# Kernel optimization log

Hardware: AMD Instinct MI355X
Metric: run time of the kernel (lower is better)

The kernel has to match this reference:

```python
import jax, jax.numpy as jnp
import numpy as np

D, H, FF, EPS = 1024, 16, 4096, 1e-5

def _ln(x, g, b):
    m = jnp.mean(x, axis=-1, keepdims=True)
    v = jnp.var(x, axis=-1, keepdims=True)
    return (x - m) * jax.lax.rsqrt(v + EPS) * g + b

def setup_inputs() -> dict:
    key = jax.random.key(0)
    ks = jax.random.split(key, 8)
    b, t = 2, 2048
    return {
        "x": jax.random.normal(ks[0], (b, t, D), jnp.float32),
        "prev_attn": jax.random.normal(ks[1], (b, H, t, t), jnp.float32) * 0.1,
        "w_qkv": jax.random.normal(ks[2], (D, 3 * D), jnp.float32) * (D ** -0.5),
        "w_out": jax.random.normal(ks[3], (D, D), jnp.float32) * (D ** -0.5),
        "w1": jax.random.normal(ks[4], (D, FF), jnp.float32) * (D ** -0.5),
        "b1": jnp.zeros((FF,), jnp.float32),
        "w2": jax.random.normal(ks[5], (FF, D), jnp.float32) * (FF ** -0.5),
        "b2": jnp.zeros((D,), jnp.float32),
        "g1": jnp.ones((D,), jnp.float32),
        "be1": jnp.zeros((D,), jnp.float32),
        "g2": jnp.ones((D,), jnp.float32),
        "be2": jnp.zeros((D,), jnp.float32),
    }

def reference(x, prev_attn, w_qkv, w_out, w1, b1, w2, b2, g1, be1, g2, be2):
    b, t, d = x.shape
    h, hd = H, d // H
    scale = hd ** -0.5
    qkv = _ln(x, g1, be1) @ w_qkv                       # [b,t,3d]
    q, k, v = jnp.split(qkv, 3, axis=-1)
    q, k, v = [z.reshape(b, t, h, hd).transpose(0, 2, 1, 3) for z in (q, k, v)]
    attn = jnp.einsum('bhid,bhjd->bhij', q, k) * scale + prev_attn
    attn = jax.nn.softmax(attn, axis=-1)                # [b,h,t,t]
    out = jnp.einsum('bhij,bhjd->bhid', attn, v).transpose(0, 2, 1, 3).reshape(b, t, d)
    x = x + out @ w_out
    hdn = _ln(x, g2, be2)
    ffn = jax.nn.gelu(hdn @ w1 + b1, approximate=False) @ w2 + b2
    x = x + ffn
    return (x, jax.lax.stop_gradient(attn))
```

## Files before the change

### kernel.cpp

```cpp
#include <hip/hip_runtime.h>
#include <hip/hip_bf16.h>
#include <math.h>

#define T_SEQ 2048
#define D_MODEL 1024
#define N_HEADS 16
#define HD 64
#define FF_DIM 4096
#define N_ROWS 4096
#define LDQKV 3072

typedef __bf16 bf16x8 __attribute__((ext_vector_type(8)));
typedef float f32x4 __attribute__((ext_vector_type(4)));

__device__ __forceinline__ unsigned short f2bf(float f) {
  union { float f; unsigned u; } v; v.f = f;
  unsigned r = v.u + 0x7FFFu + ((v.u >> 16) & 1u);
  return (unsigned short)(r >> 16);
}
__device__ __forceinline__ float bf2f(unsigned short u) {
  union { unsigned u; float f; } v; v.u = ((unsigned)u) << 16;
  return v.f;
}

__device__ __forceinline__ void gld_lds16(const void* g, void* l) {
  __builtin_amdgcn_global_load_lds(
      (const __attribute__((address_space(1))) unsigned int*)g,
      (__attribute__((address_space(3))) unsigned int*)l, 16, 0, 0);
}

__global__ __launch_bounds__(256) void transpose_w(const float* __restrict__ src,
                                                   unsigned short* __restrict__ dst,
                                                   int R, int C) {
  __shared__ float tile[32][33];
  int c0 = blockIdx.x * 32, r0 = blockIdx.y * 32;
  int tx = threadIdx.x & 31, ty = threadIdx.x >> 5;
#pragma unroll
  for (int i = 0; i < 32; i += 8)
    tile[ty + i][tx] = src[(size_t)(r0 + ty + i) * C + c0 + tx];
  __syncthreads();
#pragma unroll
  for (int i = 0; i < 32; i += 8)
    dst[(size_t)(c0 + ty + i) * R + r0 + tx] = f2bf(tile[tx][ty + i]);
}

__global__ __launch_bounds__(256) void ln_kernel(const float* __restrict__ x,
                                                 const float* __restrict__ g,
                                                 const float* __restrict__ be,
                                                 unsigned short* __restrict__ out) {
  int row = blockIdx.x;
  float4 v = ((const float4*)(x + (size_t)row * D_MODEL))[threadIdx.x];
  float s = v.x + v.y + v.z + v.w;
  float ss = v.x * v.x + v.y * v.y + v.z * v.z + v.w * v.w;
#pragma unroll
  for (int o = 32; o; o >>= 1) { s += __shfl_down(s, o); ss += __shfl_down(ss, o); }
  __shared__ float red[8];
  int wid = threadIdx.x >> 6, lane = threadIdx.x & 63;
  if (lane == 0) { red[wid] = s; red[4 + wid] = ss; }
  __syncthreads();
  if (threadIdx.x == 0) {
    float S0 = red[0] + red[1] + red[2] + red[3];
    float S1 = red[4] + red[5] + red[6] + red[7];
    float m = S0 * (1.0f / D_MODEL);
    red[0] = m;
    red[1] = rsqrtf(S1 * (1.0f / D_MODEL) - m * m + 1e-5f);
  }
  __syncthreads();
  float m = red[0], inv = red[1];
  float4 gv = ((const float4*)g)[threadIdx.x];
  float4 bv = ((const float4*)be)[threadIdx.x];
  ushort4 o;
  o.x = f2bf((v.x - m) * inv * gv.x + bv.x);
  o.y = f2bf((v.y - m) * inv * gv.y + bv.y);
  o.z = f2bf((v.z - m) * inv * gv.z + bv.z);
  o.w = f2bf((v.w - m) * inv * gv.w + bv.w);
  ((ushort4*)(out + (size_t)row * D_MODEL))[threadIdx.x] = o;
}

template <int EPI>
__global__ __launch_bounds__(256) void gemm_bt(const unsigned short* __restrict__ A,
                                               const unsigned short* __restrict__ Bt,
                                               int M, int N, int K,
                                               void* __restrict__ outp,
                                               const float* __restrict__ bias,
                                               const float* __restrict__ res) {
  __shared__ __align__(16) unsigned short As[128 * 32];
  __shared__ __align__(16) unsigned short Bs[128 * 32];
  int tid = threadIdx.x;
  int m0 = blockIdx.x * 128, n0 = blockIdx.y * 128;
  int w = tid >> 6, l = tid & 63;
  int wm = w >> 1, wn = w & 1;
  int lr = l & 15, lg = l >> 4;
  f32x4 acc[4][4] = {};
  const unsigned short* ap0 = A + (size_t)(m0 + (tid >> 2)) * K + (tid & 3) * 8;
  const unsigned short* ap1 = ap0 + (size_t)64 * K;
  const unsigned short* bp0 = Bt + (size_t)(n0 + (tid >> 2)) * K + (tid & 3) * 8;
  const unsigned short* bp1 = bp0 + (size_t)64 * K;
  unsigned short* la0 = As + (tid & ~63) * 8;
  unsigned short* la1 = As + (256 + (tid & ~63)) * 8;
  unsigned short* lb0 = Bs + (tid & ~63) * 8;
  unsigned short* lb1 = Bs + (256 + (tid & ~63)) * 8;
  for (int k0 = 0; k0 < K; k0 += 32) {
    gld_lds16(ap0, la0);
    gld_lds16(ap1, la1);
    gld_lds16(bp0, lb0);
    gld_lds16(bp1, lb1);
    ap0 += 32; ap1 += 32; bp0 += 32; bp1 += 32;
    __syncthreads();
    bf16x8 af[4], bfr[4];
#pragma unroll
    for (int i = 0; i < 4; i++) {
      af[i] = *(const bf16x8*)(As + (wm * 64 + i * 16 + lr) * 32 + lg * 8);
      bfr[i] = *(const bf16x8*)(Bs + (wn * 64 + i * 16 + lr) * 32 + lg * 8);
    }
#pragma unroll
    for (int i = 0; i < 4; i++)
#pragma unroll
      for (int j = 0; j < 4; j++)
        acc[i][j] = __builtin_amdgcn_mfma_f32_16x16x32_bf16(af[i], bfr[j], acc[i][j], 0, 0, 0);
    __syncthreads();
  }
#pragma unroll
  for (int i = 0; i < 4; i++) {
#pragma unroll
    for (int j = 0; j < 4; j++) {
      int col = n0 + wn * 64 + j * 16 + lr;
#pragma unroll
      for (int r = 0; r < 4; r++) {
        int row = m0 + wm * 64 + i * 16 + lg * 4 + r;
        size_t idx = (size_t)row * N + col;
        float v = acc[i][j][r];
        if (EPI == 0) {
          ((unsigned short*)outp)[idx] = f2bf(v);
        } else if (EPI == 1) {
          ((float*)outp)[idx] = res[idx] + v;
        } else if (EPI == 2) {
          float t = v + bias[col];
          ((unsigned short*)outp)[idx] = f2bf(0.5f * t * (1.0f + erff(t * 0.70710678f)));
        } else {
          ((float*)outp)[idx] = v + bias[col] + res[idx];
        }
      }
    }
  }
}

__global__ __launch_bounds__(256) void repack_kv(const unsigned short* __restrict__ qkv,
                                                 unsigned short* __restrict__ kt,
                                                 unsigned short* __restrict__ vt2) {
  __shared__ unsigned short tile[64][66];
  int bh = blockIdx.x >> 5, tt = blockIdx.x & 31;
  int b = bh >> 4, h = bh & 15;
  int t0 = tt * 64;
  int tid = threadIdx.x;
  const unsigned short* ksrc = qkv + (size_t)(b * T_SEQ + t0) * LDQKV + D_MODEL + h * HD;
  unsigned short* kdst = kt + ((size_t)bh * T_SEQ + t0) * HD;
#pragma unroll
  for (int i = 0; i < 16; i++) {
    int e = i * 256 + tid;
    int tr = e >> 6, d = e & 63;
    kdst[(size_t)tr * HD + d] = ksrc[(size_t)tr * LDQKV + d];
  }
  const unsigned short* vsrc = qkv + (size_t)(b * T_SEQ + t0) * LDQKV + 2 * D_MODEL + h * HD;
#pragma unroll
  for (int i = 0; i < 16; i++) {
    int e = i * 256 + tid;
    int tr = e >> 6, d = e & 63;
    tile[tr][d] = vsrc[(size_t)tr * LDQKV + d];
  }
  __syncthreads();
  unsigned short* vdst = vt2 + (size_t)bh * 64 * HD * 32 + (size_t)(t0 >> 5) * HD * 32;
#pragma unroll
  for (int i = 0; i < 16; i++) {
    int e = i * 256 + tid;
    int d = e >> 6, tr = e & 63;
    vdst[(size_t)((tr >> 5) * HD + d) * 32 + (tr & 31)] = tile[tr][d];
  }
}

__global__ __launch_bounds__(512, 4) void attn_kernel(const unsigned short* __restrict__ qkv,
                                                      const unsigned short* __restrict__ kt,
                                                      const unsigned short* __restrict__ vt2,
                                                      const float* __restrict__ prev,
                                                      float* __restrict__ attn_out,
                                                      unsigned short* __restrict__ ctx) {
  __shared__ __align__(16) unsigned short S[16 * 2048];
  int bid = blockIdx.x;
  int nb = (bid & 7) * 512 + (bid >> 3);
  int bh = nb >> 7, rt = nb & 127;
  int b = bh >> 4, h = bh & 15;
  int r0 = rt * 16;
  int tid = threadIdx.x, w = tid >> 6, l = tid & 63;
  int lr = l & 15, lg = l >> 4;

  const unsigned short* qb = qkv + (size_t)(b * T_SEQ + r0 + lr) * LDQKV + h * HD + lg * 8;
  bf16x8 qf0 = *(const bf16x8*)(qb);
  bf16x8 qf1 = *(const bf16x8*)(qb + 32);
#pragma unroll
  for (int i = 0; i < 8; i++) {
    qf0[i] = (__bf16)((float)qf0[i] * 0.125f);
    qf1[i] = (__bf16)((float)qf1[i] * 0.125f);
  }

  const unsigned short* kb0 = kt + (size_t)bh * T_SEQ * HD + lg * 8;
#pragma unroll
  for (int nt = 0; nt < 16; nt++) {
    int c = w * 256 + nt * 16 + lr;
    const unsigned short* kp = kb0 + (size_t)c * HD;
    bf16x8 kf0 = *(const bf16x8*)(kp);
    bf16x8 kf1 = *(const bf16x8*)(kp + 32);
    f32x4 a = {};
    a = __builtin_amdgcn_mfma_f32_16x16x32_bf16(qf0, kf0, a, 0, 0, 0);
    a = __builtin_amdgcn_mfma_f32_16x16x32_bf16(qf1, kf1, a, 0, 0, 0);
#pragma unroll
    for (int r = 0; r < 4; r++) {
      int row = lg * 4 + r;
      int byteoff = (c * 2) ^ ((row & 7) << 4);
      *(unsigned short*)((char*)S + row * 4096 + byteoff) = f2bf(a[r]);
    }
  }
  __syncthreads();

  const float* pvb = prev + ((size_t)bh * T_SEQ + r0 + 2 * w) * T_SEQ;
  float* arow0 = attn_out + ((size_t)bh * T_SEQ + r0 + 2 * w) * T_SEQ;
#pragma unroll
  for (int rr = 0; rr < 2; rr++) {
    int row = w * 2 + rr;
    char* Sr = (char*)S + row * 4096;
    int xv = (row & 7) << 4;
    const float* pr = pvb + (size_t)rr * T_SEQ;
    float* ar = arow0 + (size_t)rr * T_SEQ;
    f32x4 sv[8];
    float mx = -1e30f;
#pragma unroll
    for (int i = 0; i < 8; i++) {
      int c = l * 4 + i * 256;
      ushort4 sraw = *(const ushort4*)(Sr + ((2 * c) ^ xv));
      f32x4 p = *(const f32x4*)(pr + c);
      sv[i][0] = bf2f(sraw.x) + p[0];
      sv[i][1] = bf2f(sraw.y) + p[1];
      sv[i][2] = bf2f(sraw.z) + p[2];
      sv[i][3] = bf2f(sraw.w) + p[3];
      mx = fmaxf(mx, fmaxf(fmaxf(sv[i][0], sv[i][1]), fmaxf(sv[i][2], sv[i][3])));
    }
#pragma unroll
    for (int o = 32; o; o >>= 1) mx = fmaxf(mx, __shfl_xor(mx, o));
    float sum = 0.f;
#pragma unroll
    for (int i = 0; i < 8; i++) {
      sv[i][0] = __expf(sv[i][0] - mx);
      sv[i][1] = __expf(sv[i][1] - mx);
      sv[i][2] = __expf(sv[i][2] - mx);
      sv[i][3] = __expf(sv[i][3] - mx);
      sum += sv[i][0] + sv[i][1] + sv[i][2] + sv[i][3];
    }
#pragma unroll
    for (int o = 32; o; o >>= 1) sum += __shfl_xor(sum, o);
    float inv = 1.0f / sum;
#pragma unroll
    for (int i = 0; i < 8; i++) {
      int c = l * 4 + i * 256;
      float4 p4;
      p4.x = sv[i][0] * inv; p4.y = sv[i][1] * inv;
      p4.z = sv[i][2] * inv; p4.w = sv[i][3] * inv;
      *(float4*)(ar + c) = p4;
      ushort4 pbf;
      pbf.x = f2bf(p4.x); pbf.y = f2bf(p4.y); pbf.z = f2bf(p4.z); pbf.w = f2bf(p4.w);
      *(ushort4*)(Sr + ((2 * c) ^ xv)) = pbf;
    }
  }
  __syncthreads();

  f32x4 pacc[4] = {};
  const unsigned short* vb = vt2 + (size_t)bh * 64 * HD * 32;
#pragma unroll
  for (int kt_i = 0; kt_i < 8; kt_i++) {
    int kb = w * 256 + kt_i * 32;
    char* Sr = (char*)S + lr * 4096;
    int byteoff = ((kb + lg * 8) * 2) ^ ((lr & 7) << 4);
    bf16x8 af = *(const bf16x8*)(Sr + byteoff);
    const unsigned short* vtile = vb + (size_t)(kb >> 5) * HD * 32;
#pragma unroll
    for (int nj = 0; nj < 4; nj++) {
      const unsigned short* vp = vtile + (size_t)(nj * 16 + lr) * 32 + lg * 8;
      bf16x8 bv = *(const bf16x8*)(vp);
      pacc[nj] = __builtin_amdgcn_mfma_f32_16x16x32_bf16(af, bv, pacc[nj], 0, 0, 0);
    }
  }
  __syncthreads();

  float* P = (float*)S;
#pragma unroll
  for (int nj = 0; nj < 4; nj++)
#pragma unroll
    for (int r = 0; r < 4; r++)
      P[(w * 16 + lg * 4 + r) * 64 + nj * 16 + lr] = pacc[nj][r];
  __syncthreads();
  for (int e = tid; e < 1024; e += 512) {
    float s = 0.f;
#pragma unroll
    for (int ww = 0; ww < 8; ww++) s += P[ww * 1024 + e];
    int row = e >> 6, col = e & 63;
    ctx[(size_t)(b * T_SEQ + r0 + row) * D_MODEL + h * HD + col] = f2bf(s);
  }
}

extern "C" void kernel_launch(void* const* d_in, const int* in_sizes, int n_in,
                              void* d_out, int out_size, void* d_ws, size_t ws_size,
                              hipStream_t stream) {
  const float* x = (const float*)d_in[0];
  const float* prev = (const float*)d_in[1];
  const float* w_qkv = (const float*)d_in[2];
  const float* w_out = (const float*)d_in[3];
  const float* w1 = (const float*)d_in[4];
  const float* b1 = (const float*)d_in[5];
  const float* w2 = (const float*)d_in[6];
  const float* b2 = (const float*)d_in[7];
  const float* g1 = (const float*)d_in[8];
  const float* be1 = (const float*)d_in[9];
  const float* g2 = (const float*)d_in[10];
  const float* be2 = (const float*)d_in[11];
  float* out_x = (float*)d_out;
  float* out_attn = out_x + (size_t)N_ROWS * D_MODEL;

  char* p = (char*)d_ws;
  auto alloc = [&](size_t bytes) -> void* {
    void* r = (void*)p;
    p += (bytes + 255) & ~(size_t)255;
    return r;
  };
  unsigned short* wqkvT = (unsigned short*)alloc((size_t)3072 * 1024 * 2);
  unsigned short* woutT = (unsigned short*)alloc((size_t)1024 * 1024 * 2);
  unsigned short* w1T   = (unsigned short*)alloc((size_t)4096 * 1024 * 2);
  unsigned short* w2T   = (unsigned short*)alloc((size_t)1024 * 4096 * 2);
  unsigned short* ln1b  = (unsigned short*)alloc((size_t)N_ROWS * 1024 * 2);
  unsigned short* qkvb  = (unsigned short*)alloc((size_t)N_ROWS * 3072 * 2);
  unsigned short* ktb   = (unsigned short*)alloc((size_t)32 * 2048 * 64 * 2);
  unsigned short* vt2b  = (unsigned short*)alloc((size_t)32 * 64 * 64 * 32 * 2);
  unsigned short* ctxb  = (unsigned short*)alloc((size_t)N_ROWS * 1024 * 2);
  float*          x2b   = (float*)alloc((size_t)N_ROWS * 1024 * 4);
  unsigned short* ln2b  = (unsigned short*)alloc((size_t)N_ROWS * 1024 * 2);
  unsigned short* hb    = (unsigned short*)alloc((size_t)N_ROWS * 4096 * 2);

  transpose_w<<<dim3(3072 / 32, 1024 / 32), 256, 0, stream>>>(w_qkv, wqkvT, 1024, 3072);
  transpose_w<<<dim3(1024 / 32, 1024 / 32), 256, 0, stream>>>(w_out, woutT, 1024, 1024);
  transpose_w<<<dim3(4096 / 32, 1024 / 32), 256, 0, stream>>>(w1, w1T, 1024, 4096);
  transpose_w<<<dim3(1024 / 32, 4096 / 32), 256, 0, stream>>>(w2, w2T, 4096, 1024);

  ln_kernel<<<N_ROWS, 256, 0, stream>>>(x, g1, be1, ln1b);
  gemm_bt<0><<<dim3(32, 24), 256, 0, stream>>>(ln1b, wqkvT, N_ROWS, 3072, 1024, qkvb, nullptr, nullptr);
  repack_kv<<<32 * 32, 256, 0, stream>>>(qkvb, ktb, vt2b);
  attn_kernel<<<32 * 128, 512, 0, stream>>>(qkvb, ktb, vt2b, prev, out_attn, ctxb);
  gemm_bt<1><<<dim3(32, 8), 256, 0, stream>>>(ctxb, woutT, N_ROWS, 1024, 1024, x2b, nullptr, x);
  ln_kernel<<<N_ROWS, 256, 0, stream>>>(x2b, g2, be2, ln2b);
  gemm_bt<2><<<dim3(32, 32), 256, 0, stream>>>(ln2b, w1T, N_ROWS, 4096, 1024, hb, b1, nullptr);
  gemm_bt<3><<<dim3(32, 8), 256, 0, stream>>>(hb, w2T, N_ROWS, 1024, 4096, out_x, b2, x2b);
}
```

Baseline: 603.4 us.

## Use smaller-tile GEMM for N=1024 projections, fold Q scale into QKV epilogue

Adds a 64x128-tile GEMM variant (gemm_bt2) for the output projection and FFN down-projection. With N=1024 the old tiling launched only 256 blocks, and the smaller tile doubles that to 512 to fill more of the GPU's compute units. The 1/sqrt(hd) query scaling moves from the attention kernel into the QKV GEMM epilogue, and s_setprio hints are wrapped around the MFMA sections in attention. The cost is less data reuse per block in the smaller-tile GEMM and slightly different bf16 rounding for the pre-scaled Q.

```diff
diff --git a/kernel.cpp b/kernel.cpp
--- a/kernel.cpp
+++ b/kernel.cpp
@@ -131,12 +131,75 @@
         size_t idx = (size_t)row * N + col;
         float v = acc[i][j][r];
         if (EPI == 0) {
+          if (col < 1024) v *= 0.125f;
           ((unsigned short*)outp)[idx] = f2bf(v);
-        } else if (EPI == 1) {
-          ((float*)outp)[idx] = res[idx] + v;
         } else if (EPI == 2) {
           float t = v + bias[col];
           ((unsigned short*)outp)[idx] = f2bf(0.5f * t * (1.0f + erff(t * 0.70710678f)));
+        }
+      }
+    }
+  }
+}
+
+template <int EPI>
+__global__ __launch_bounds__(256) void gemm_bt2(const unsigned short* __restrict__ A,
+                                                const unsigned short* __restrict__ Bt,
+                                                int M, int N, int K,
+                                                void* __restrict__ outp,
+                                                const float* __restrict__ bias,
+                                                const float* __restrict__ res) {
+  __shared__ __align__(16) unsigned short As[64 * 64];
+  __shared__ __align__(16) unsigned short Bs[128 * 64];
+  int tid = threadIdx.x;
+  int m0 = blockIdx.x * 64, n0 = blockIdx.y * 128;
+  int w = tid >> 6, l = tid & 63;
+  int lr = l & 15, lg = l >> 4;
+  f32x4 acc[4][2] = {};
+  int srow = tid >> 3;
+  int scolb = ((tid & 7) * 16) ^ ((srow & 7) << 4);
+  const unsigned short* apg = A + (size_t)(m0 + srow) * K + (scolb >> 1);
+  const unsigned short* bpg = Bt + (size_t)(n0 + srow) * K + (scolb >> 1);
+  unsigned short* la = As + tid * 8;
+  unsigned short* lb = Bs + tid * 8;
+  for (int k0 = 0; k0 < K; k0 += 64) {
+    gld_lds16(apg + k0, la);
+    gld_lds16(apg + (size_t)32 * K + k0, la + 32 * 64);
+    gld_lds16(bpg + k0, lb);
+    gld_lds16(bpg + (size_t)32 * K + k0, lb + 32 * 64);
+    gld_lds16(bpg + (size_t)64 * K + k0, lb + 64 * 64);
+    gld_lds16(bpg + (size_t)96 * K + k0, lb + 96 * 64);
+    __syncthreads();
+#pragma unroll
+    for (int kk = 0; kk < 2; kk++) {
+      int cb = (lg * 16 + kk * 64) ^ ((lr & 7) << 4);
+      bf16x8 af[4], bfr[2];
+#pragma unroll
+      for (int i = 0; i < 4; i++)
+        af[i] = *(const bf16x8*)((const char*)As + (i * 16 + lr) * 128 + cb);
+#pragma unroll
+      for (int j = 0; j < 2; j++)
+        bfr[j] = *(const bf16x8*)((const char*)Bs + (w * 32 + j * 16 + lr) * 128 + cb);
+#pragma unroll
+      for (int i = 0; i < 4; i++)
+#pragma unroll
+        for (int j = 0; j < 2; j++)
+          acc[i][j] = __builtin_amdgcn_mfma_f32_16x16x32_bf16(af[i], bfr[j], acc[i][j], 0, 0, 0);
+    }
+    __syncthreads();
+  }
+#pragma unroll
+  for (int i = 0; i < 4; i++) {
+#pragma unroll
+    for (int j = 0; j < 2; j++) {
+      int col = n0 + w * 32 + j * 16 + lr;
+#pragma unroll
+      for (int r = 0; r < 4; r++) {
+        int row = m0 + i * 16 + lg * 4 + r;
+        size_t idx = (size_t)row * N + col;
+        float v = acc[i][j][r];
+        if (EPI == 1) {
+          ((float*)outp)[idx] = res[idx] + v;
         } else {
           ((float*)outp)[idx] = v + bias[col] + res[idx];
         }
@@ -196,11 +259,6 @@
   const unsigned short* qb = qkv + (size_t)(b * T_SEQ + r0 + lr) * LDQKV + h * HD + lg * 8;
   bf16x8 qf0 = *(const bf16x8*)(qb);
   bf16x8 qf1 = *(const bf16x8*)(qb + 32);
-#pragma unroll
-  for (int i = 0; i < 8; i++) {
-    qf0[i] = (__bf16)((float)qf0[i] * 0.125f);
-    qf1[i] = (__bf16)((float)qf1[i] * 0.125f);
-  }
 
   const unsigned short* kb0 = kt + (size_t)bh * T_SEQ * HD + lg * 8;
 #pragma unroll
@@ -210,8 +268,10 @@
     bf16x8 kf0 = *(const bf16x8*)(kp);
     bf16x8 kf1 = *(const bf16x8*)(kp + 32);
     f32x4 a = {};
+    __builtin_amdgcn_s_setprio(1);
     a = __builtin_amdgcn_mfma_f32_16x16x32_bf16(qf0, kf0, a, 0, 0, 0);
     a = __builtin_amdgcn_mfma_f32_16x16x32_bf16(qf1, kf1, a, 0, 0, 0);
+    __builtin_amdgcn_s_setprio(0);
 #pragma unroll
     for (int r = 0; r < 4; r++) {
       int row = lg * 4 + r;
@@ -280,12 +340,14 @@
     int byteoff = ((kb + lg * 8) * 2) ^ ((lr & 7) << 4);
     bf16x8 af = *(const bf16x8*)(Sr + byteoff);
     const unsigned short* vtile = vb + (size_t)(kb >> 5) * HD * 32;
+    __builtin_amdgcn_s_setprio(1);
 #pragma unroll
     for (int nj = 0; nj < 4; nj++) {
       const unsigned short* vp = vtile + (size_t)(nj * 16 + lr) * 32 + lg * 8;
       bf16x8 bv = *(const bf16x8*)(vp);
       pacc[nj] = __builtin_amdgcn_mfma_f32_16x16x32_bf16(af, bv, pacc[nj], 0, 0, 0);
     }
+    __builtin_amdgcn_s_setprio(0);
   }
   __syncthreads();
 
@@ -351,8 +413,8 @@
   gemm_bt<0><<<dim3(32, 24), 256, 0, stream>>>(ln1b, wqkvT, N_ROWS, 3072, 1024, qkvb, nullptr, nullptr);
   repack_kv<<<32 * 32, 256, 0, stream>>>(qkvb, ktb, vt2b);
   attn_kernel<<<32 * 128, 512, 0, stream>>>(qkvb, ktb, vt2b, prev, out_attn, ctxb);
-  gemm_bt<1><<<dim3(32, 8), 256, 0, stream>>>(ctxb, woutT, N_ROWS, 1024, 1024, x2b, nullptr, x);
+  gemm_bt2<1><<<dim3(64, 8), 256, 0, stream>>>(ctxb, woutT, N_ROWS, 1024, 1024, x2b, nullptr, x);
   ln_kernel<<<N_ROWS, 256, 0, stream>>>(x2b, g2, be2, ln2b);
   gemm_bt<2><<<dim3(32, 32), 256, 0, stream>>>(ln2b, w1T, N_ROWS, 4096, 1024, hb, b1, nullptr);
-  gemm_bt<3><<<dim3(32, 8), 256, 0, stream>>>(hb, w2T, N_ROWS, 1024, 4096, out_x, b2, x2b);
-}
+  gemm_bt2<3><<<dim3(64, 8), 256, 0, stream>>>(hb, w2T, N_ROWS, 1024, 4096, out_x, b2, x2b);
+}
```

Result: faster. 587.1 us (-2.7%).
